# Performance work log

Hardware: AMD Instinct MI355X
Metric: run time of the kernel (lower is better)

## Reference

```python
import jax, jax.numpy as jnp
import numpy as np

GRID_SIZE = 8
POS_LAMBDA = 250.0
POS_MARGIN = 1.0
NEG_MARGIN = 0.2


def setup_inputs() -> dict:
    key = jax.random.key(0)
    k1, k2, k3, k4 = jax.random.split(key, 4)
    N, C, Hr, Wr = 8, 128, 30, 40
    H, W = Hr * GRID_SIZE, Wr * GRID_SIZE
    des1 = jax.random.normal(k1, (N, C, Hr, Wr), jnp.float32)
    des2 = jax.random.normal(k2, (N, C, Hr, Wr), jnp.float32)
    # near-identity homography so the positive-pair mask s is non-trivial
    homo = jnp.eye(3, dtype=jnp.float32) + 0.001 * jax.random.normal(k3, (3, 3), jnp.float32)
    mask = (jax.random.uniform(k4, (N, 1, H, W)) > 0.05).astype(jnp.float32)
    return {"des1": des1, "des2": des2, "homo": homo, "mask": mask}


def reference(des1, des2, homo, mask):
    n, c, hr, wr = des1.shape
    gs = GRID_SIZE

    # coordinate grid of cell centers in full-res pixel coords: (x, y)
    ys, xs = jnp.meshgrid(jnp.arange(hr), jnp.arange(wr), indexing='ij')
    grid = jnp.stack([xs, ys], axis=-1).astype(homo.dtype) * gs + gs // 2  # Hr,Wr,2
    grid = jnp.broadcast_to(grid, (n, hr, wr, 2))

    # warp grid by homography
    gh = jnp.concatenate([grid, jnp.ones((n, hr, wr, 1), homo.dtype)], axis=-1)  # N,Hr,Wr,3
    wg = jnp.einsum('nhwk,jk->nhwj', gh, homo)
    w_grid = wg[..., :2] / wg[..., 2:3]  # N,Hr,Wr,2

    # pairwise distance between grid cells of img1 and warped cells of img2
    diff = grid[:, :, :, None, None, :] - w_grid[:, None, None, :, :, :]  # N,Hr,Wr,Hr,Wr,2
    grid_dist = jnp.sqrt(jnp.sum(diff * diff, axis=-1))                   # N,Hr,Wr,Hr,Wr
    s = (grid_dist <= gs - 0.5).astype(des1.dtype)

    # dense descriptor cross-correlation (contraction over channels)
    dot_des = jnp.einsum('ncij,nckl->nijkl', des1, des2)  # N,Hr,Wr,Hr,Wr

    pos_dist = jnp.maximum(POS_MARGIN - dot_des, 0.0)
    neg_dist = jnp.maximum(dot_des - NEG_MARGIN, 0.0)
    loss = POS_LAMBDA * s * pos_dist + (1.0 - s) * neg_dist

    # space_to_depth(mask, gs).prod(dim=1)
    m = mask.reshape(n, 1, hr, gs, wr, gs)
    r_mask = jnp.prod(m, axis=(1, 3, 5))            # N,Hr,Wr
    r_mask5 = r_mask.reshape(n, 1, 1, hr, wr)

    norm = hr * wr * jnp.sum(r_mask5)
    loss = jnp.sum(loss * r_mask5) / norm
    return (loss, s, dot_des, r_mask5[:, 0])  # r_mask squeezed -> N,1,Hr,Wr
```

## Files before the change

kernel.cpp:

```cpp
#include <hip/hip_runtime.h>
#include <hip/hip_bf16.h>

#define HRr 30
#define WRr 40
#define MM 1200
#define CC 128
#define NB 8
#define GS 8

constexpr int PT = 19;
constexpr int TILE_SH = 16 * 64 * 8;
constexpr int NPART = 2400;

typedef __attribute__((ext_vector_type(8))) short bf16x8;
typedef __attribute__((ext_vector_type(4))) float f32x4;

__device__ inline short f2bf(float f) {
    union { float f; unsigned u; } v; v.f = f;
    unsigned r = v.u + 0x7FFFu + ((v.u >> 16) & 1u);
    return (short)(r >> 16);
}

__global__ __launch_bounds__(256) void convert_prep_kernel(const float* __restrict__ des1,
                                                           const float* __restrict__ des2,
                                                           const float* __restrict__ homo,
                                                           const float* __restrict__ mask,
                                                           short* __restrict__ wsA,
                                                           short* __restrict__ wsB,
                                                           float2* __restrict__ wgrid,
                                                           float* __restrict__ out_rmask,
                                                           float* __restrict__ ws_rmask) {
    const int t     = threadIdx.x;
    const int ptile = blockIdx.x;
    const int n     = blockIdx.z;

    if (blockIdx.y == 0) {
        const int gid = (blockIdx.z * gridDim.x + blockIdx.x) * 256 + t;
        if (gid < MM) {
            int k = gid / WRr, l = gid % WRr;
            float x = (float)(l * GS + GS / 2);
            float y = (float)(k * GS + GS / 2);
            float nx = homo[0] * x + homo[1] * y + homo[2];
            float ny = homo[3] * x + homo[4] * y + homo[5];
            float dn = homo[6] * x + homo[7] * y + homo[8];
            wgrid[gid] = make_float2(nx / dn, ny / dn);
        }
        if (gid < NB * MM) {
            int nn = gid / MM;
            int rem = gid % MM;
            int k = rem / WRr, l = rem % WRr;
            const float* mp = mask + (size_t)nn * (240 * 320) + (size_t)(k * GS) * 320 + l * GS;
            float prod = 1.f;
            #pragma unroll
            for (int yy = 0; yy < GS; ++yy) {
                float4 a = *reinterpret_cast<const float4*>(&mp[yy * 320]);
                float4 b = *reinterpret_cast<const float4*>(&mp[yy * 320 + 4]);
                prod *= a.x * a.y * a.z * a.w * b.x * b.y * b.z * b.w;
            }
            out_rmask[gid] = prod;
            ws_rmask[gid]  = prod;
        }
    }

    const int lane = t & 63;
    const int g    = t >> 6;
    const int p    = ptile * 64 + lane;
    const int kr   = blockIdx.y * 2 + (g >> 1);
    const int kb   = kr * 8;
    const int isB  = g & 1;

    const float* src = (isB ? des2 : des1) + (size_t)n * CC * MM;
    short* dst = (isB ? wsB : wsA) + (size_t)(n * PT + ptile) * TILE_SH;

    bf16x8 wv;
    #pragma unroll
    for (int i = 0; i < 8; ++i) {
        float v = (p < MM) ? src[(size_t)(kb + i) * MM + p] : 0.f;
        wv[i] = f2bf(v);
    }
    const int rb = lane >> 4, lc = lane & 15;
    const int ks = kr >> 2, lrk = kr & 3;
    const size_t off = (size_t)(((ks * 4 + rb) * 64) + lrk * 16 + lc) * 8;
    *reinterpret_cast<bf16x8*>(&dst[off]) = wv;
}

__global__ __launch_bounds__(256) void main_kernel(const short* __restrict__ wsA,
                                                   const short* __restrict__ wsB,
                                                   const float2* __restrict__ wgrid,
                                                   const float* __restrict__ rmask,
                                                   float* __restrict__ out_s,
                                                   float* __restrict__ out_dot,
                                                   float* __restrict__ partials) {
    __shared__ float Ds[16 * 308];
    __shared__ float red[4];

    const int f   = blockIdx.x;
    const int lid = (f & 7) * 300 + (f >> 3);
    const int n       = lid / 300;
    const int rem     = lid % 300;
    const int strip   = rem >> 2;
    const int quarter = rem & 3;
    const int p0    = strip * 16;
    const int cbase = quarter * 304;
    const int nf    = (quarter < 3) ? 19 : 18;
    const int W     = (quarter < 3) ? 304 : 288;
    const int fbase = quarter * 19;

    const int t    = threadIdx.x;
    const int lane = t & 63;
    const int w    = t >> 6;
    const int lr   = lane >> 4, lc = lane & 15;

    const short* An  = wsA + (size_t)(n * PT + (p0 >> 6)) * TILE_SH;
    const int    rbA = (p0 >> 4) & 3;
    bf16x8 af[4];
    #pragma unroll
    for (int ks = 0; ks < 4; ++ks)
        af[ks] = *reinterpret_cast<const bf16x8*>(&An[(size_t)(((ks * 4 + rbA) * 64) + lane) * 8]);

    const short* Bn = wsB + (size_t)n * PT * TILE_SH;
    const float* rm = rmask + n * MM;

    for (int i = w; i < nf; i += 4) {
        const int g = fbase + i;
        const short* Bt = Bn + (size_t)(g >> 2) * TILE_SH;
        const int rbB = g & 3;
        f32x4 acc = {0.f, 0.f, 0.f, 0.f};
        #pragma unroll
        for (int ks = 0; ks < 4; ++ks) {
            bf16x8 bfr = *reinterpret_cast<const bf16x8*>(
                &Bt[(size_t)(((ks * 4 + rbB) * 64) + lane) * 8]);
            acc = __builtin_amdgcn_mfma_f32_16x16x32_bf16(af[ks], bfr, acc, 0, 0, 0);
        }
        #pragma unroll
        for (int r = 0; r < 4; ++r)
            Ds[(lr * 4 + r) * 308 + 1 + i * 16 + lc] = acc[r];
    }
    __syncthreads();

    const int row = t >> 4;
    const int l16 = t & 15;
    const int p   = p0 + row;
    const float gx = (float)((p % WRr) * GS + GS / 2);
    const float gy = (float)((p / WRr) * GS + GS / 2);
    const size_t rowbase = (size_t)(n * MM + p) * MM;
    const float* dsr = &Ds[row * 308 + 1];
    const int h = 31 - 16 * (p & 1);
    const int cAl = (((h - cbase) % 32) + 32) % 32;

    float a0 = 0.f, a1 = 0.f, a2 = 0.f, a3 = 0.f;

    for (int c = l16; c < cAl; c += 16) {
        const float dot = dsr[c];
        const int q = cbase + c;
        const float2 wg = wgrid[q];
        const float dx = gx - wg.x, dy = gy - wg.y;
        const float d2 = dx * dx + dy * dy;
        const float s = (d2 <= 56.25f) ? 1.f : 0.f;
        const float le = 250.f * s * fmaxf(1.f - dot, 0.f) + (1.f - s) * fmaxf(dot - 0.2f, 0.f);
        a0 += le * rm[q];
        out_dot[rowbase + q] = dot;
        out_s[rowbase + q] = s;
    }
    const int nl = (W - cAl) >> 5;
    const int s4 = nl << 3;
    const int ts = cAl + (nl << 5);
    for (int k = 0;; ++k) {
        const int jj = l16 + (k << 4);
        if (jj >= s4) break;
        const int c = cAl + (jj << 2);
        const int q = cbase + c;
        const f32x4 dv = *reinterpret_cast<const f32x4*>(&dsr[c]);
        f32x4 sv;
        {
            const float2 wg0 = wgrid[q];
            const float2 wg1 = wgrid[q + 1];
            const float2 wg2 = wgrid[q + 2];
            const float2 wg3 = wgrid[q + 3];
            const float dx0 = gx - wg0.x, dy0 = gy - wg0.y;
            const float dx1 = gx - wg1.x, dy1 = gy - wg1.y;
            const float dx2 = gx - wg2.x, dy2 = gy - wg2.y;
            const float dx3 = gx - wg3.x, dy3 = gy - wg3.y;
            sv[0] = (dx0 * dx0 + dy0 * dy0 <= 56.25f) ? 1.f : 0.f;
            sv[1] = (dx1 * dx1 + dy1 * dy1 <= 56.25f) ? 1.f : 0.f;
            sv[2] = (dx2 * dx2 + dy2 * dy2 <= 56.25f) ? 1.f : 0.f;
            sv[3] = (dx3 * dx3 + dy3 * dy3 <= 56.25f) ? 1.f : 0.f;
        }
        const float le0 = 250.f * sv[0] * fmaxf(1.f - dv[0], 0.f) + (1.f - sv[0]) * fmaxf(dv[0] - 0.2f, 0.f);
        const float le1 = 250.f * sv[1] * fmaxf(1.f - dv[1], 0.f) + (1.f - sv[1]) * fmaxf(dv[1] - 0.2f, 0.f);
        const float le2 = 250.f * sv[2] * fmaxf(1.f - dv[2], 0.f) + (1.f - sv[2]) * fmaxf(dv[2] - 0.2f, 0.f);
        const float le3 = 250.f * sv[3] * fmaxf(1.f - dv[3], 0.f) + (1.f - sv[3]) * fmaxf(dv[3] - 0.2f, 0.f);
        a0 += le0 * rm[q];
        a1 += le1 * rm[q + 1];
        a2 += le2 * rm[q + 2];
        a3 += le3 * rm[q + 3];
        *reinterpret_cast<f32x4*>(&out_dot[rowbase + q]) = dv;
        *reinterpret_cast<f32x4*>(&out_s[rowbase + q]) = sv;
    }
    for (int c = ts + l16; c < W; c += 16) {
        const float dot = dsr[c];
        const int q = cbase + c;
        const float2 wg = wgrid[q];
        const float dx = gx - wg.x, dy = gy - wg.y;
        const float d2 = dx * dx + dy * dy;
        const float s = (d2 <= 56.25f) ? 1.f : 0.f;
        const float le = 250.f * s * fmaxf(1.f - dot, 0.f) + (1.f - s) * fmaxf(dot - 0.2f, 0.f);
        a1 += le * rm[q];
        out_dot[rowbase + q] = dot;
        out_s[rowbase + q] = s;
    }

    float lsum = (a0 + a1) + (a2 + a3);

    #pragma unroll
    for (int off = 32; off > 0; off >>= 1)
        lsum += __shfl_xor(lsum, off, 64);
    if (lane == 0) red[w] = lsum;
    __syncthreads();
    if (t == 0)
        partials[lid] = (red[0] + red[1]) + (red[2] + red[3]);
}

__global__ __launch_bounds__(1024) void final_kernel(const float* __restrict__ partials,
                                                     const float* __restrict__ rmask,
                                                     float* __restrict__ out_loss) {
    __shared__ float r1[16], r2[16];
    const int t = threadIdx.x;
    const int lane = t & 63;
    const int w = t >> 6;

    float s1 = 0.f, s2 = 0.f;
    for (int i = t; i < NPART; i += 1024) s1 += partials[i];
    for (int i = t; i < NB * MM; i += 1024) s2 += rmask[i];
    #pragma unroll
    for (int off = 32; off > 0; off >>= 1) {
        s1 += __shfl_xor(s1, off, 64);
        s2 += __shfl_xor(s2, off, 64);
    }
    if (lane == 0) { r1[w] = s1; r2[w] = s2; }
    __syncthreads();
    if (t == 0) {
        float total = 0.f, rsum = 0.f;
        #pragma unroll
        for (int i = 0; i < 16; ++i) { total += r1[i]; rsum += r2[i]; }
        out_loss[0] = total / ((float)MM * rsum);
    }
}

extern "C" void kernel_launch(void* const* d_in, const int* in_sizes, int n_in,
                              void* d_out, int out_size, void* d_ws, size_t ws_size,
                              hipStream_t stream) {
    const float* des1 = (const float*)d_in[0];
    const float* des2 = (const float*)d_in[1];
    const float* homo = (const float*)d_in[2];
    const float* mask = (const float*)d_in[3];

    float* out      = (float*)d_out;
    float* out_loss = out;
    float* out_s    = out + 1;
    float* out_dot  = out + 1 + (size_t)NB * MM * MM;
    float* out_rm   = out + 1 + 2 * (size_t)NB * MM * MM;

    char* wsb = (char*)d_ws;
    float2* wgrid    = (float2*)(wsb);
    float*  partials = (float*)(wsb + 16384);
    float*  ws_rm    = (float*)(wsb + 32768);
    short*  wsA      = (short*)(wsb + 131072);
    short*  wsB      = wsA + (size_t)NB * PT * TILE_SH;

    dim3 cgrid(PT, 8, NB);
    convert_prep_kernel<<<cgrid, 256, 0, stream>>>(des1, des2, homo, mask,
                                                   wsA, wsB, wgrid, out_rm, ws_rm);

    main_kernel<<<dim3(NPART, 1, 1), 256, 0, stream>>>(wsA, wsB, wgrid, ws_rm,
                                                       out_s, out_dot, partials);

    final_kernel<<<1, 1024, 0, stream>>>(partials, ws_rm, out_loss);
}
```

Baseline: 38.77 us.

## Fuse final reduction into main kernel via atomic ticket and halve column tiles

```diff
diff --git a/kernel.cpp b/kernel.cpp
--- a/kernel.cpp
+++ b/kernel.cpp
@@ -10,7 +10,7 @@
 
 constexpr int PT = 19;
 constexpr int TILE_SH = 16 * 64 * 8;
-constexpr int NPART = 2400;
+constexpr int NTASK = 4800;
 
 typedef __attribute__((ext_vector_type(8))) short bf16x8;
 typedef __attribute__((ext_vector_type(4))) float f32x4;
@@ -29,10 +29,17 @@
                                                            short* __restrict__ wsB,
                                                            float2* __restrict__ wgrid,
                                                            float* __restrict__ out_rmask,
-                                                           float* __restrict__ ws_rmask) {
+                                                           float* __restrict__ ws_rmask,
+                                                           float* __restrict__ loss_acc,
+                                                           int* __restrict__ ticket) {
     const int t     = threadIdx.x;
     const int ptile = blockIdx.x;
     const int n     = blockIdx.z;
+
+    if (blockIdx.x == 0 && blockIdx.y == 0 && blockIdx.z == 0 && t == 0) {
+        *loss_acc = 0.f;
+        *ticket   = 0;
+    }
 
     if (blockIdx.y == 0) {
         const int gid = (blockIdx.z * gridDim.x + blockIdx.x) * 256 + t;
@@ -90,21 +97,23 @@
                                                    const float* __restrict__ rmask,
                                                    float* __restrict__ out_s,
                                                    float* __restrict__ out_dot,
-                                                   float* __restrict__ partials) {
-    __shared__ float Ds[16 * 308];
+                                                   float* __restrict__ loss_acc,
+                                                   int* __restrict__ ticket,
+                                                   float* __restrict__ out_loss) {
+    __shared__ float Ds[16 * 164];
     __shared__ float red[4];
+    __shared__ int lastFlag;
 
     const int f   = blockIdx.x;
-    const int lid = (f & 7) * 300 + (f >> 3);
-    const int n       = lid / 300;
-    const int rem     = lid % 300;
-    const int strip   = rem >> 2;
-    const int quarter = rem & 3;
-    const int p0    = strip * 16;
-    const int cbase = quarter * 304;
-    const int nf    = (quarter < 3) ? 19 : 18;
-    const int W     = (quarter < 3) ? 304 : 288;
-    const int fbase = quarter * 19;
+    const int n   = f & 7;
+    const int idx = f >> 3;
+    const int strip  = idx >> 3;
+    const int e      = idx & 7;
+    const int p0     = strip * 16;
+    const int fbase  = e * 9 + (e < 3 ? e : 3);
+    const int nf     = (e < 3) ? 10 : 9;
+    const int cbase  = fbase * 16;
+    const int W      = nf * 16;
 
     const int t    = threadIdx.x;
     const int lane = t & 63;
@@ -134,7 +143,7 @@
         }
         #pragma unroll
         for (int r = 0; r < 4; ++r)
-            Ds[(lr * 4 + r) * 308 + 1 + i * 16 + lc] = acc[r];
+            Ds[(lr * 4 + r) * 164 + 1 + i * 16 + lc] = acc[r];
     }
     __syncthreads();
 
@@ -144,7 +153,7 @@
     const float gx = (float)((p % WRr) * GS + GS / 2);
     const float gy = (float)((p / WRr) * GS + GS / 2);
     const size_t rowbase = (size_t)(n * MM + p) * MM;
-    const float* dsr = &Ds[row * 308 + 1];
+    const float* dsr = &Ds[row * 164 + 1];
     const int h = 31 - 16 * (p & 1);
     const int cAl = (((h - cbase) % 32) + 32) % 32;
 
@@ -217,33 +226,28 @@
         lsum += __shfl_xor(lsum, off, 64);
     if (lane == 0) red[w] = lsum;
     __syncthreads();
-    if (t == 0)
-        partials[lid] = (red[0] + red[1]) + (red[2] + red[3]);
-}
-
-__global__ __launch_bounds__(1024) void final_kernel(const float* __restrict__ partials,
-                                                     const float* __restrict__ rmask,
-                                                     float* __restrict__ out_loss) {
-    __shared__ float r1[16], r2[16];
-    const int t = threadIdx.x;
-    const int lane = t & 63;
-    const int w = t >> 6;
-
-    float s1 = 0.f, s2 = 0.f;
-    for (int i = t; i < NPART; i += 1024) s1 += partials[i];
-    for (int i = t; i < NB * MM; i += 1024) s2 += rmask[i];
-    #pragma unroll
-    for (int off = 32; off > 0; off >>= 1) {
-        s1 += __shfl_xor(s1, off, 64);
-        s2 += __shfl_xor(s2, off, 64);
-    }
-    if (lane == 0) { r1[w] = s1; r2[w] = s2; }
+    if (t == 0) {
+        const float bsum = (red[0] + red[1]) + (red[2] + red[3]);
+        const float old = atomicAdd(loss_acc, bsum);
+        asm volatile("" :: "v"(old));
+        const int tk = atomicAdd(ticket, 1);
+        lastFlag = (tk == NTASK - 1) ? 1 : 0;
+    }
     __syncthreads();
-    if (t == 0) {
-        float total = 0.f, rsum = 0.f;
+
+    if (lastFlag) {
+        float s2 = 0.f;
+        for (int i = t; i < NB * MM; i += 256) s2 += rmask[i];
         #pragma unroll
-        for (int i = 0; i < 16; ++i) { total += r1[i]; rsum += r2[i]; }
-        out_loss[0] = total / ((float)MM * rsum);
+        for (int off = 32; off > 0; off >>= 1)
+            s2 += __shfl_xor(s2, off, 64);
+        if (lane == 0) red[w] = s2;
+        __syncthreads();
+        if (t == 0) {
+            const float rsum  = (red[0] + red[1]) + (red[2] + red[3]);
+            const float total = atomicAdd(loss_acc, 0.0f);
+            out_loss[0] = total / ((float)MM * rsum);
+        }
     }
 }
 
@@ -263,17 +267,18 @@
 
     char* wsb = (char*)d_ws;
     float2* wgrid    = (float2*)(wsb);
-    float*  partials = (float*)(wsb + 16384);
+    float*  loss_acc = (float*)(wsb + 16384);
+    int*    ticket   = (int*)(wsb + 16384 + 64);
     float*  ws_rm    = (float*)(wsb + 32768);
     short*  wsA      = (short*)(wsb + 131072);
     short*  wsB      = wsA + (size_t)NB * PT * TILE_SH;
 
     dim3 cgrid(PT, 8, NB);
     convert_prep_kernel<<<cgrid, 256, 0, stream>>>(des1, des2, homo, mask,
-                                                   wsA, wsB, wgrid, out_rm, ws_rm);
-
-    main_kernel<<<dim3(NPART, 1, 1), 256, 0, stream>>>(wsA, wsB, wgrid, ws_rm,
-                                                       out_s, out_dot, partials);
-
-    final_kernel<<<1, 1024, 0, stream>>>(partials, ws_rm, out_loss);
-}
+                                                   wsA, wsB, wgrid, out_rm, ws_rm,
+                                                   loss_acc, ticket);
+
+    main_kernel<<<dim3(NTASK, 1, 1), 256, 0, stream>>>(wsA, wsB, wgrid, ws_rm,
+                                                       out_s, out_dot,
+                                                       loss_acc, ticket, out_loss);
+}
```

New measurement: 97.78 us. 152% more time.
